# Kernel tuning notes

Hardware: AMD Instinct MI355X
Metric: run time of the kernel (lower is better)

The kernel has to match this reference:

```python
import jax, jax.numpy as jnp
import numpy as np

K_NUM = 4      # kernel_num: size of dynamic kernel bank
KS = 3         # spatial kernel size


def _fdconv(x, w_fr, w_fi, b, a1w, a1b, a2w, a2b):
    """Frequency-dynamic conv: kernels parameterized in the Fourier domain,
    mixed per-sample by a GAP->MLP->softmax attention over the kernel bank,
    then applied as a per-sample 3x3 conv (batched via grouped conv).
    x: [B,Cin,H,W]; w_fr/w_fi: [K,Cout,Cin,3,2] (rfft2 coeffs); b: [Cout]."""
    B, Cin, H, W = x.shape
    # per-sample kernel attention
    gap = x.mean((2, 3))                                   # [B,Cin]
    h = jax.nn.relu(gap @ a1w + a1b)                       # [B,hidden]
    attn = jax.nn.softmax(h @ a2w + a2b, axis=-1)          # [B,K]
    # synthesize spatial kernels from frequency coefficients
    w = jnp.fft.irfft2(w_fr + 1j * w_fi, s=(KS, KS), axes=(-2, -1))  # [K,Co,Ci,3,3]
    w = w.astype(x.dtype)
    wd = jnp.einsum('bk,koihw->boihw', attn, w)            # [B,Co,Ci,3,3]
    Co = wd.shape[1]
    # per-sample conv via feature_group_count=B grouped conv
    xg = x.reshape(1, B * Cin, H, W)
    wg = wd.reshape(B * Co, Cin, KS, KS)
    y = jax.lax.conv_general_dilated(
        xg, wg, window_strides=(1, 1), padding='SAME',
        dimension_numbers=('NCHW', 'OIHW', 'NCHW'),
        feature_group_count=B)
    return y.reshape(B, Co, H, W) + b[None, :, None, None]


def setup_inputs() -> dict:
    key = jax.random.key(0)
    ks = jax.random.split(key, 16)
    B, Cin, Cout, H, W = 16, 128, 256, 128, 128
    h1, h2 = Cin // 4, Cout // 4
    FR = KS // 2 + 1  # rfft bins along last dim
    s = 0.05
    return {
        'x': jax.random.normal(ks[0], (B, Cin, H, W), jnp.float32),
        # conv1 (Cin->Cout)
        'w1_fr': jax.random.normal(ks[1], (K_NUM, Cout, Cin, KS, FR), jnp.float32) * s,
        'w1_fi': jax.random.normal(ks[2], (K_NUM, Cout, Cin, KS, FR), jnp.float32) * s,
        'b1': jnp.zeros((Cout,), jnp.float32),
        'a1w1': jax.random.normal(ks[3], (Cin, h1), jnp.float32) * s,
        'a1b1': jnp.zeros((h1,), jnp.float32),
        'a1w2': jax.random.normal(ks[4], (h1, K_NUM), jnp.float32) * s,
        'a1b2': jnp.zeros((K_NUM,), jnp.float32),
        # conv2 (Cout->Cout)
        'w2_fr': jax.random.normal(ks[5], (K_NUM, Cout, Cout, KS, FR), jnp.float32) * s,
        'w2_fi': jax.random.normal(ks[6], (K_NUM, Cout, Cout, KS, FR), jnp.float32) * s,
        'b2': jnp.zeros((Cout,), jnp.float32),
        'a2w1': jax.random.normal(ks[7], (Cout, h2), jnp.float32) * s,
        'a2b1': jnp.zeros((h2,), jnp.float32),
        'a2w2': jax.random.normal(ks[8], (h2, K_NUM), jnp.float32) * s,
        'a2b2': jnp.zeros((K_NUM,), jnp.float32),
    }


def reference(x, w1_fr, w1_fi, b1, a1w1, a1b1, a1w2, a1b2,
              w2_fr, w2_fi, b2, a2w1, a2b1, a2w2, a2b2):
    y = jax.nn.relu(_fdconv(x, w1_fr, w1_fi, b1, a1w1, a1b1, a1w2, a1b2))
    y = jax.nn.relu(_fdconv(y, w2_fr, w2_fi, b2, a2w1, a2b1, a2w2, a2b2))
    return y
```

## Files before the change

### kernel.cpp

```cpp
#include <hip/hip_runtime.h>
#include <hip/hip_bf16.h>
#include <math.h>


#define K_NUM 4
typedef __attribute__((ext_vector_type(8))) short short8;
typedef __attribute__((ext_vector_type(4))) float f32x4;
typedef __attribute__((ext_vector_type(16))) float f32x16;

__device__ inline float bf2f(short s) {
  unsigned u = ((unsigned)(unsigned short)s) << 16;
  return __uint_as_float(u);
}
__device__ inline short f2bf(float f) {
  __hip_bfloat16 h = __float2bfloat16(f);
  return (short)*reinterpret_cast<unsigned short*>(&h);
}

__global__ __launch_bounds__(256) void gap_reduce_kernel(
    const float* __restrict__ part, float* __restrict__ gap, float scale, int n4) {
  int row = blockIdx.x * 4 + (threadIdx.x >> 6);
  int lane = threadIdx.x & 63;
  float4 v = {0.f, 0.f, 0.f, 0.f};
  if (lane < n4) v = *(const float4*)(part + (size_t)row * 256 + lane * 4);
  float s = v.x + v.y + v.z + v.w;
#pragma unroll
  for (int m = 1; m <= 32; m <<= 1) s += __shfl_xor(s, m, 64);
  if (lane == 0) gap[row] = s * scale;
}

__global__ void fd_attn_kernel(const float* __restrict__ gap, int C, int Hd,
                               const float* __restrict__ w1, const float* __restrict__ b1,
                               const float* __restrict__ w2, const float* __restrict__ b2,
                               float* __restrict__ attn) {
  int b = blockIdx.x, j = threadIdx.x;
  __shared__ float h[64];
  __shared__ float z[K_NUM];
  if (j < Hd) {
    float s = b1[j];
    const float* g = gap + (size_t)b * C;
    for (int c = 0; c < C; ++c) s = fmaf(g[c], w1[c * Hd + j], s);
    h[j] = fmaxf(s, 0.f);
  }
  __syncthreads();
  if (j < K_NUM) {
    float s = b2[j];
    for (int c = 0; c < Hd; ++c) s = fmaf(h[c], w2[c * K_NUM + j], s);
    z[j] = s;
  }
  __syncthreads();
  if (j == 0) {
    float m = z[0];
    for (int k = 1; k < K_NUM; ++k) m = fmaxf(m, z[k]);
    float e[K_NUM], sum = 0.f;
    for (int k = 0; k < K_NUM; ++k) { e[k] = expf(z[k] - m); sum += e[k]; }
    for (int k = 0; k < K_NUM; ++k) attn[b * K_NUM + k] = e[k] / sum;
  }
}

__global__ void fd_synth_t_kernel(const float* __restrict__ wfr, const float* __restrict__ wfi,
                                  const float* __restrict__ attn, short* __restrict__ wdt,
                                  int B, int CO, int CI) {
  size_t gid = (size_t)blockIdx.x * blockDim.x + threadIdx.x;
  size_t total = (size_t)B * CI * CO;
  if (gid >= total) return;
  int ci = (int)(gid % CI);
  size_t t = gid / CI;
  int co = (int)(t % CO);
  int b = (int)(t / CO);

  float a[K_NUM];
  for (int k = 0; k < K_NUM; ++k) a[k] = attn[b * K_NUM + k];

  float Fr[3][2], Fi[3][2];
  for (int u = 0; u < 3; ++u) for (int v = 0; v < 2; ++v) { Fr[u][v] = 0.f; Fi[u][v] = 0.f; }
  for (int k = 0; k < K_NUM; ++k) {
    size_t base = ((((size_t)k * CO + co) * CI + ci) * 3) * 2;
    const float* pr = wfr + base;
    const float* pi = wfi + base;
    float ak = a[k];
    for (int u = 0; u < 3; ++u)
      for (int v = 0; v < 2; ++v) {
        Fr[u][v] = fmaf(ak, pr[u * 2 + v], Fr[u][v]);
        Fi[u][v] = fmaf(ak, pi[u * 2 + v], Fi[u][v]);
      }
  }

  const float CS[3] = {1.f, -0.5f, -0.5f};
  const float SN[3] = {0.f, 0.8660254037844386f, -0.8660254037844386f};
  float outv[9];
  for (int ai = 0; ai < 3; ++ai) {
    float Gr[2], Gi[2];
    for (int v = 0; v < 2; ++v) {
      float gr = 0.f, gi = 0.f;
      for (int u = 0; u < 3; ++u) {
        int idx = (u * ai) % 3;
        gr += Fr[u][v] * CS[idx] - Fi[u][v] * SN[idx];
        gi += Fr[u][v] * SN[idx] + Fi[u][v] * CS[idx];
      }
      Gr[v] = gr * (1.f / 3.f);
      Gi[v] = gi * (1.f / 3.f);
    }
    for (int bi = 0; bi < 3; ++bi)
      outv[ai * 3 + bi] = (Gr[0] + 2.f * (Gr[1] * CS[bi] - Gi[1] * SN[bi])) * (1.f / 3.f);
  }
  int ci8 = ci >> 3, cil = ci & 7;
  for (int s = 0; s < 9; ++s)
    wdt[((((size_t)b * 9 + s) * (CI / 8) + ci8) * CO + co) * 8 + cil] = f2bf(outv[s]);
}

__global__ __launch_bounds__(256) void transpose_bf16_kernel(
    const float* __restrict__ in, short* __restrict__ out, int C,
    float* __restrict__ gpart1) {
  const int HW = 16384;
  __shared__ short t[64 * 40];
  int tid = threadIdx.x;
  int px0 = blockIdx.x * 64, c0 = blockIdx.y * 32, b = blockIdx.z;
  int px = tid & 63, cb = tid >> 6;
  float sums[8];
#pragma unroll
  for (int i = 0; i < 8; ++i) {
    int c = i * 4 + cb;
    float v = in[((size_t)b * C + c0 + c) * HW + px0 + px];
    t[px * 40 + c] = f2bf(v);
    sums[i] = v;
  }
  __syncthreads();
  int px2 = tid >> 2, g = tid & 3;
  short8 v = *(const short8*)(t + px2 * 40 + g * 8);
  *(short8*)(out + ((size_t)b * HW + px0 + px2) * C + c0 + g * 8) = v;
#pragma unroll
  for (int m = 1; m <= 32; m <<= 1)
#pragma unroll
    for (int i = 0; i < 8; ++i) sums[i] += __shfl_xor(sums[i], m, 64);
  if ((tid & 63) == 0)
#pragma unroll
    for (int i = 0; i < 8; ++i)
      gpart1[((size_t)b * C + c0 + i * 4 + cb) * 256 + blockIdx.x] = sums[i];
}

template <int CI, int MODE>
__global__ __launch_bounds__(512, 2) void conv_mfma_kernel(
    const short* __restrict__ xin,
    const short* __restrict__ wdt,
    const float* __restrict__ bias,
    short* __restrict__ yout_t,
    float* __restrict__ yout_f,
    float* __restrict__ gpart2) {
  const int H = 128, W = 128, HW = H * W, CO = 256;
  const int NKC = CI / 32;
  const int NPX = 340;
  const int NPXP = 346;
  __shared__ short xs[2][4 * NPXP * 8];

  const int tid = threadIdx.x;
  const int w = tid >> 6;
  const int wy = w & 1, wc = w >> 1;
  const int lane = tid & 63;
  const int l31 = lane & 31;
  const int h = lane >> 5;
  const int tx0 = (blockIdx.x & 3) * 32, ty0 = (blockIdx.x >> 2) * 8;
  const int cob = wc * 64;
  const int b = blockIdx.z;

  const int sp = tid;
  const int srr = sp / 34, scc = sp - srr * 34;
  const int sgy = ty0 + srr - 1, sgx = tx0 + scc - 1;
  const bool sok = (tid < NPX);
  const bool sin = sok && (unsigned)sgy < (unsigned)H && (unsigned)sgx < (unsigned)W;
  const short* sgp = xin + ((size_t)b * HW + sgy * W + sgx) * CI;

  short8 pre[4];
  auto stage_load = [&](int kc) {
#pragma unroll
    for (int g = 0; g < 4; ++g) {
      short8 v = {0, 0, 0, 0, 0, 0, 0, 0};
      if (sin) v = *(const short8*)(sgp + kc * 32 + g * 8);
      pre[g] = v;
    }
  };
  auto stage_write = [&](short* buf) {
    if (sok) {
#pragma unroll
      for (int g = 0; g < 4; ++g)
        *(short8*)(buf + (g * NPXP + sp) * 8) = pre[g];
    }
  };

  f32x16 acc[4][2];
#pragma unroll
  for (int i = 0; i < 4; ++i)
#pragma unroll
    for (int j = 0; j < 2; ++j)
#pragma unroll
      for (int r = 0; r < 16; ++r) acc[i][j][r] = 0.f;

  stage_load(0);
  stage_write(xs[0]);
  __syncthreads();

  int cur = 0;
  for (int kc = 0; kc < NKC; ++kc) {
    const bool more = (kc + 1 < NKC);
    if (more) stage_load(kc + 1);
    const short* bufc = xs[cur];

#pragma unroll
    for (int dc = 0; dc < 3; ++dc) {
#pragma unroll
      for (int ks = 0; ks < 2; ++ks) {
        short8 xf[6];
#pragma unroll
        for (int rr = 0; rr < 6; ++rr) {
          int p = (wy * 4 + rr) * 34 + l31 + dc;
          xf[rr] = *(const short8*)(bufc + ((ks * 2 + h) * NPXP + p) * 8);
        }
#pragma unroll
        for (int dr = 0; dr < 3; ++dr) {
          short8 wf[2];
          const short* wp = wdt + ((((size_t)b * 9 + dr * 3 + dc) * (CI / 8) + kc * 4 + ks * 2 + h) * CO + cob + l31) * 8;
#pragma unroll
          for (int ncf = 0; ncf < 2; ++ncf)
            wf[ncf] = *(const short8*)(wp + ncf * 32 * 8);
#pragma unroll
          for (int nf = 0; nf < 4; ++nf)
#pragma unroll
            for (int ncf = 0; ncf < 2; ++ncf) {
              if (MODE == 0)
                acc[nf][ncf] = __builtin_amdgcn_mfma_f32_32x32x16_bf16(
                    xf[nf + dr], wf[ncf], acc[nf][ncf], 0, 0, 0);
              else
                acc[nf][ncf] = __builtin_amdgcn_mfma_f32_32x32x16_bf16(
                    wf[ncf], xf[nf + dr], acc[nf][ncf], 0, 0, 0);
            }
        }
      }
    }

    if (more) stage_write(xs[cur ^ 1]);
    __syncthreads();
    cur ^= 1;
  }

  if (MODE == 0) {
    float gs[2] = {0.f, 0.f};
#pragma unroll
    for (int ncf = 0; ncf < 2; ++ncf) {
      int co = cob + ncf * 32 + l31;
      float bs = bias[co];
#pragma unroll
      for (int nf = 0; nf < 4; ++nf) {
        int row = ty0 + wy * 4 + nf;
#pragma unroll
        for (int reg = 0; reg < 16; ++reg) {
          int mcol = (reg & 3) + 8 * (reg >> 2) + 4 * h;
          int col = tx0 + mcol;
          float v = fmaxf(acc[nf][ncf][reg] + bs, 0.f);
          gs[ncf] += v;
          yout_t[((size_t)b * HW + (size_t)row * W + col) * CO + co] = f2bf(v);
        }
      }
    }
#pragma unroll
    for (int ncf = 0; ncf < 2; ++ncf) gs[ncf] += __shfl_xor(gs[ncf], 32, 64);
    if (lane < 32) {
      int pslot = blockIdx.x * 2 + wy;
#pragma unroll
      for (int ncf = 0; ncf < 2; ++ncf)
        gpart2[((size_t)b * 256 + cob + ncf * 32 + lane) * 256 + pslot] = gs[ncf];
    }
  } else {
#pragma unroll
    for (int ncf = 0; ncf < 2; ++ncf) {
#pragma unroll
      for (int reg = 0; reg < 16; ++reg) {
        int co = cob + ncf * 32 + (reg & 3) + 8 * (reg >> 2) + 4 * h;
        float bs = bias[co];
#pragma unroll
        for (int nf = 0; nf < 4; ++nf) {
          int row = ty0 + wy * 4 + nf;
          yout_f[((size_t)b * CO + co) * HW + (size_t)row * W + tx0 + l31] =
              fmaxf(acc[nf][ncf][reg] + bs, 0.f);
        }
      }
    }
  }
}

extern "C" void kernel_launch(void* const* d_in, const int* in_sizes, int n_in,
                              void* d_out, int out_size, void* d_ws, size_t ws_size,
                              hipStream_t stream) {
  const int B = 16, CIN = 128, COUT = 256, H = 128, W = 128, HW = H * W;

  const float* x    = (const float*)d_in[0];
  const float* w1fr = (const float*)d_in[1];
  const float* w1fi = (const float*)d_in[2];
  const float* b1   = (const float*)d_in[3];
  const float* a1w1 = (const float*)d_in[4];
  const float* a1b1 = (const float*)d_in[5];
  const float* a1w2 = (const float*)d_in[6];
  const float* a1b2 = (const float*)d_in[7];
  const float* w2fr = (const float*)d_in[8];
  const float* w2fi = (const float*)d_in[9];
  const float* b2   = (const float*)d_in[10];
  const float* a2w1 = (const float*)d_in[11];
  const float* a2b1 = (const float*)d_in[12];
  const float* a2w2 = (const float*)d_in[13];
  const float* a2b2 = (const float*)d_in[14];
  float* outf = (float*)d_out;

  short* xt     = (short*)d_out;
  float* gpart1 = (float*)((char*)d_out + 67108864);
  float* gpart2 = (float*)((char*)d_out + 69206016);

  char* wsb = (char*)d_ws;
  short* y1t  = (short*)wsb;
  short* wdt  = (short*)(wsb + 134217728);
  float* gap1 = (float*)(wsb + 134217728 + 18874368);
  float* gap2 = (float*)(wsb + 134217728 + 18874368 + 8192);
  float* attn = (float*)(wsb + 134217728 + 18874368 + 8192 + 16384);

  const float gsc = 1.f / (float)HW;

  transpose_bf16_kernel<<<dim3(HW / 64, CIN / 32, B), 256, 0, stream>>>(x, xt, CIN, gpart1);
  gap_reduce_kernel<<<(B * CIN) / 4, 256, 0, stream>>>(gpart1, gap1, gsc, 64);
  fd_attn_kernel<<<B, 64, 0, stream>>>(gap1, CIN, CIN / 4, a1w1, a1b1, a1w2, a1b2, attn);
  fd_synth_t_kernel<<<(B * CIN * COUT) / 256, 256, 0, stream>>>(w1fr, w1fi, attn, wdt, B, COUT, CIN);
  conv_mfma_kernel<128, 0><<<dim3(64, 1, 16), 512, 0, stream>>>(xt, wdt, b1, y1t, nullptr, gpart2);

  gap_reduce_kernel<<<(B * COUT) / 4, 256, 0, stream>>>(gpart2, gap2, gsc, 32);
  fd_attn_kernel<<<B, 64, 0, stream>>>(gap2, COUT, COUT / 4, a2w1, a2b1, a2w2, a2b2, attn);
  fd_synth_t_kernel<<<(B * COUT * COUT) / 256, 256, 0, stream>>>(w2fr, w2fi, attn, wdt, B, COUT, COUT);
  conv_mfma_kernel<256, 1><<<dim3(64, 1, 16), 512, 0, stream>>>(y1t, wdt, b2, nullptr, outf, nullptr);
}
```

Before: 1.015 ms.

## Use direct global-to-LDS loads and double-buffer weight fragments in conv kernel

Replaces the register-staged input tile copy (global load into registers, then LDS store) with global_load_lds DMA-style loads, using a zeroed scratch buffer as the source for padding pixels. Also restructures the inner loop so the weight fragments for the next (dc,ks) step are prefetched into a second register set while the current step's MFMAs run. The goal is to cut VGPR pressure and LDS store instructions and to hide weight-load latency behind the MFMAs. The risks are more live registers from the double-buffered weights, and relying on correct wave-base LDS addressing for global_load_lds.

Result: faster. 988.0 us (-2.7%).

```diff
diff --git a/kernel.cpp b/kernel.cpp
--- a/kernel.cpp
+++ b/kernel.cpp
@@ -15,6 +15,10 @@
 __device__ inline short f2bf(float f) {
   __hip_bfloat16 h = __float2bfloat16(f);
   return (short)*reinterpret_cast<unsigned short*>(&h);
+}
+
+__device__ inline void gll16(const void* g, void* l) {
+  __builtin_amdgcn_global_load_lds(g, l, 16, 0, 0);
 }
 
 __global__ __launch_bounds__(256) void gap_reduce_kernel(
@@ -146,7 +150,8 @@
     const float* __restrict__ bias,
     short* __restrict__ yout_t,
     float* __restrict__ yout_f,
-    float* __restrict__ gpart2) {
+    float* __restrict__ gpart2,
+    const short* __restrict__ zbuf) {
   const int H = 128, W = 128, HW = H * W, CO = 256;
   const int NKC = CI / 32;
   const int NPX = 340;
@@ -168,23 +173,28 @@
   const int sgy = ty0 + srr - 1, sgx = tx0 + scc - 1;
   const bool sok = (tid < NPX);
   const bool sin = sok && (unsigned)sgy < (unsigned)H && (unsigned)sgx < (unsigned)W;
-  const short* sgp = xin + ((size_t)b * HW + sgy * W + sgx) * CI;
-
-  short8 pre[4];
-  auto stage_load = [&](int kc) {
-#pragma unroll
-    for (int g = 0; g < 4; ++g) {
-      short8 v = {0, 0, 0, 0, 0, 0, 0, 0};
-      if (sin) v = *(const short8*)(sgp + kc * 32 + g * 8);
-      pre[g] = v;
+  const short* sgp = xin + ((size_t)b * HW + (size_t)sgy * W + sgx) * CI;
+  const int wbase = tid & ~63;
+
+  auto stage_issue = [&](int kc, int buf) {
+    if (sok) {
+#pragma unroll
+      for (int g = 0; g < 4; ++g) {
+        const void* src = sin ? (const void*)(sgp + kc * 32 + g * 8) : (const void*)zbuf;
+        void* dst = (void*)(xs[buf] + (g * NPXP + wbase) * 8);
+        gll16(src, dst);
+      }
     }
   };
-  auto stage_write = [&](short* buf) {
-    if (sok) {
-#pragma unroll
-      for (int g = 0; g < 4; ++g)
-        *(short8*)(buf + (g * NPXP + sp) * 8) = pre[g];
-    }
+
+  const size_t drs = (size_t)3 * (CI / 8) * CO * 8;
+  auto load_wf = [&](short8 wfb[6], int kc, int dc, int ks) {
+    const short* wp = wdt + ((((size_t)b * 9 + dc) * (CI / 8) + kc * 4 + ks * 2 + h) * CO + cob + l31) * 8;
+#pragma unroll
+    for (int dr = 0; dr < 3; ++dr)
+#pragma unroll
+      for (int ncf = 0; ncf < 2; ++ncf)
+        wfb[dr * 2 + ncf] = *(const short8*)(wp + dr * drs + ncf * 256);
   };
 
   f32x16 acc[4][2];
@@ -195,49 +205,47 @@
 #pragma unroll
       for (int r = 0; r < 16; ++r) acc[i][j][r] = 0.f;
 
-  stage_load(0);
-  stage_write(xs[0]);
+  short8 wfp[2][6];
+
+  stage_issue(0, 0);
+  load_wf(wfp[0], 0, 0, 0);
   __syncthreads();
 
   int cur = 0;
   for (int kc = 0; kc < NKC; ++kc) {
     const bool more = (kc + 1 < NKC);
-    if (more) stage_load(kc + 1);
+    if (more) stage_issue(kc + 1, cur ^ 1);
     const short* bufc = xs[cur];
 
 #pragma unroll
-    for (int dc = 0; dc < 3; ++dc) {
-#pragma unroll
-      for (int ks = 0; ks < 2; ++ks) {
-        short8 xf[6];
-#pragma unroll
-        for (int rr = 0; rr < 6; ++rr) {
-          int p = (wy * 4 + rr) * 34 + l31 + dc;
-          xf[rr] = *(const short8*)(bufc + ((ks * 2 + h) * NPXP + p) * 8);
-        }
-#pragma unroll
-        for (int dr = 0; dr < 3; ++dr) {
-          short8 wf[2];
-          const short* wp = wdt + ((((size_t)b * 9 + dr * 3 + dc) * (CI / 8) + kc * 4 + ks * 2 + h) * CO + cob + l31) * 8;
-#pragma unroll
-          for (int ncf = 0; ncf < 2; ++ncf)
-            wf[ncf] = *(const short8*)(wp + ncf * 32 * 8);
-#pragma unroll
-          for (int nf = 0; nf < 4; ++nf)
-#pragma unroll
-            for (int ncf = 0; ncf < 2; ++ncf) {
-              if (MODE == 0)
-                acc[nf][ncf] = __builtin_amdgcn_mfma_f32_32x32x16_bf16(
-                    xf[nf + dr], wf[ncf], acc[nf][ncf], 0, 0, 0);
-              else
-                acc[nf][ncf] = __builtin_amdgcn_mfma_f32_32x32x16_bf16(
-                    wf[ncf], xf[nf + dr], acc[nf][ncf], 0, 0, 0);
-            }
-        }
-      }
-    }
-
-    if (more) stage_write(xs[cur ^ 1]);
+    for (int g = 0; g < 6; ++g) {
+      const int dc = g >> 1, ks = g & 1;
+      if (g < 5)
+        load_wf(wfp[(g + 1) & 1], kc, (g + 1) >> 1, (g + 1) & 1);
+      else if (more)
+        load_wf(wfp[(g + 1) & 1], kc + 1, 0, 0);
+
+      short8 xf[6];
+#pragma unroll
+      for (int rr = 0; rr < 6; ++rr) {
+        int p = (wy * 4 + rr) * 34 + l31 + dc;
+        xf[rr] = *(const short8*)(bufc + ((ks * 2 + h) * NPXP + p) * 8);
+      }
+#pragma unroll
+      for (int dr = 0; dr < 3; ++dr)
+#pragma unroll
+        for (int nf = 0; nf < 4; ++nf)
+#pragma unroll
+          for (int ncf = 0; ncf < 2; ++ncf) {
+            if (MODE == 0)
+              acc[nf][ncf] = __builtin_amdgcn_mfma_f32_32x32x16_bf16(
+                  xf[nf + dr], wfp[g & 1][dr * 2 + ncf], acc[nf][ncf], 0, 0, 0);
+            else
+              acc[nf][ncf] = __builtin_amdgcn_mfma_f32_32x32x16_bf16(
+                  wfp[g & 1][dr * 2 + ncf], xf[nf + dr], acc[nf][ncf], 0, 0, 0);
+          }
+    }
+
     __syncthreads();
     cur ^= 1;
   }
@@ -316,20 +324,23 @@
   char* wsb = (char*)d_ws;
   short* y1t  = (short*)wsb;
   short* wdt  = (short*)(wsb + 134217728);
-  float* gap1 = (float*)(wsb + 134217728 + 18874368);
-  float* gap2 = (float*)(wsb + 134217728 + 18874368 + 8192);
-  float* attn = (float*)(wsb + 134217728 + 18874368 + 8192 + 16384);
+  float* gap1 = (float*)(wsb + 153092096);
+  float* gap2 = (float*)(wsb + 153100288);
+  float* attn = (float*)(wsb + 153116672);
+  short* zbuf = (short*)(wsb + 153116928);
 
   const float gsc = 1.f / (float)HW;
+
+  hipMemsetAsync(zbuf, 0, 256, stream);
 
   transpose_bf16_kernel<<<dim3(HW / 64, CIN / 32, B), 256, 0, stream>>>(x, xt, CIN, gpart1);
   gap_reduce_kernel<<<(B * CIN) / 4, 256, 0, stream>>>(gpart1, gap1, gsc, 64);
   fd_attn_kernel<<<B, 64, 0, stream>>>(gap1, CIN, CIN / 4, a1w1, a1b1, a1w2, a1b2, attn);
   fd_synth_t_kernel<<<(B * CIN * COUT) / 256, 256, 0, stream>>>(w1fr, w1fi, attn, wdt, B, COUT, CIN);
-  conv_mfma_kernel<128, 0><<<dim3(64, 1, 16), 512, 0, stream>>>(xt, wdt, b1, y1t, nullptr, gpart2);
+  conv_mfma_kernel<128, 0><<<dim3(64, 1, 16), 512, 0, stream>>>(xt, wdt, b1, y1t, nullptr, gpart2, zbuf);
 
   gap_reduce_kernel<<<(B * COUT) / 4, 256, 0, stream>>>(gpart2, gap2, gsc, 32);
   fd_attn_kernel<<<B, 64, 0, stream>>>(gap2, COUT, COUT / 4, a2w1, a2b1, a2w2, a2b2, attn);
   fd_synth_t_kernel<<<(B * COUT * COUT) / 256, 256, 0, stream>>>(w2fr, w2fi, attn, wdt, B, COUT, COUT);
-  conv_mfma_kernel<256, 1><<<dim3(64, 1, 16), 512, 0, stream>>>(y1t, wdt, b2, nullptr, outf, nullptr);
-}
+  conv_mfma_kernel<256, 1><<<dim3(64, 1, 16), 512, 0, stream>>>(y1t, wdt, b2, nullptr, outf, nullptr, zbuf);
+}
```
